# Kernel tuning notes

Measured on AMD Instinct MI355X. Metric: run time of the kernel, lower is better.

Reference implementation:

```python
import jax, jax.numpy as jnp
import numpy as np
import math

IMG = 640.0
SIZES = [32.0, 64.0, 128.0, 256.0]
STRIDES = [4, 8, 16, 32]
ARS = [0.5, 1.0, 2.0]
PRE_TOPK = 1000      # RPN_PRE_NMS_TOPK_TEST
POST_TOPK = 150      # RPN_POST_NMS_TOPK_TEST
NMS_THR = 0.7        # RPN_NMS_THRESHOLD
MIN_SIZE = 4.0       # MIN_BOX_SIZE
BBOX_CLAMP = math.log(1000.0 / 16.0)
ROI_OUT = 7          # ROI_OUTPUT_SIZE


def conv(x, w, b, pad):
    y = jax.lax.conv_general_dilated(x, w, (1, 1), [(pad, pad), (pad, pad)],
                                     dimension_numbers=('NCHW', 'OIHW', 'NCHW'))
    return y + b[None, :, None, None]


def level_anchors(H, W, stride, size):
    sx = (jnp.arange(W, dtype=jnp.float32) + 0.5) * stride
    sy = (jnp.arange(H, dtype=jnp.float32) + 0.5) * stride
    SY, SX = jnp.meshgrid(sy, sx, indexing='ij')
    shifts = jnp.stack([SX, SY, SX, SY], axis=-1).reshape(-1, 4)  # [H*W,4]
    base = []
    area = size * size
    for ar in ARS:
        w = math.sqrt(area / ar)
        h = ar * w
        base.append([-w / 2.0, -h / 2.0, w / 2.0, h / 2.0])
    base = jnp.asarray(base, jnp.float32)  # [3,4]
    return (shifts[:, None, :] + base[None, :, :]).reshape(-1, 4)  # [H*W*3,4]


def decode(deltas, boxes):
    w = jnp.maximum(boxes[:, 2] - boxes[:, 0], 1e-6)
    h = jnp.maximum(boxes[:, 3] - boxes[:, 1], 1e-6)
    cx = boxes[:, 0] + 0.5 * w
    cy = boxes[:, 1] + 0.5 * h
    dx, dy = deltas[:, 0], deltas[:, 1]
    dw = jnp.minimum(deltas[:, 2], BBOX_CLAMP)
    dh = jnp.minimum(deltas[:, 3], BBOX_CLAMP)
    pcx = cx + dx * w
    pcy = cy + dy * h
    pw = w * jnp.exp(dw)
    ph = h * jnp.exp(dh)
    return jnp.stack([pcx - 0.5 * pw, pcy - 0.5 * ph, pcx + 0.5 * pw, pcy + 0.5 * ph], axis=1)


def pairwise_iou(b):
    area = jnp.maximum(b[:, 2] - b[:, 0], 0) * jnp.maximum(b[:, 3] - b[:, 1], 0)
    lt = jnp.maximum(b[:, None, :2], b[None, :, :2])
    rb = jnp.minimum(b[:, None, 2:], b[None, :, 2:])
    wh = jnp.maximum(rb - lt, 0.0)
    inter = wh[..., 0] * wh[..., 1]
    return inter / jnp.maximum(area[:, None] + area[None, :] - inter, 1e-6)


def roi_align(feat, boxes, scale):
    # feat [C,H,W]; boxes [R,4] in image coords; one bilinear sample per bin center
    C, H, W = feat.shape
    b = boxes * scale
    x1, y1, x2, y2 = b[:, 0], b[:, 1], b[:, 2], b[:, 3]
    bw = jnp.maximum(x2 - x1, 1.0)
    bh = jnp.maximum(y2 - y1, 1.0)
    g = (jnp.arange(ROI_OUT, dtype=jnp.float32) + 0.5) / ROI_OUT
    px = x1[:, None] + g[None, :] * bw[:, None]   # [R,7]
    py = y1[:, None] + g[None, :] * bh[:, None]
    Y = jnp.broadcast_to(py[:, :, None], (py.shape[0], ROI_OUT, ROI_OUT))
    X = jnp.broadcast_to(px[:, None, :], (px.shape[0], ROI_OUT, ROI_OUT))
    y0f = jnp.floor(Y)
    x0f = jnp.floor(X)
    ly = Y - y0f
    lx = X - x0f
    y0 = jnp.clip(y0f, 0, H - 1).astype(jnp.int32)
    y1i = jnp.clip(y0f + 1, 0, H - 1).astype(jnp.int32)
    x0 = jnp.clip(x0f, 0, W - 1).astype(jnp.int32)
    x1i = jnp.clip(x0f + 1, 0, W - 1).astype(jnp.int32)
    f = lambda yi, xi: feat[:, yi, xi]  # [C,R,7,7]
    val = (f(y0, x0) * (1 - ly) * (1 - lx) + f(y0, x1i) * (1 - ly) * lx
           + f(y1i, x0) * ly * (1 - lx) + f(y1i, x1i) * ly * lx)
    return val.transpose(1, 0, 2, 3)  # [R,C,7,7]


def _forward(p2, p3, p4, p5, rpn_conv_w, rpn_conv_b, obj_w, obj_b, delta_w, delta_b,
             fc1_w, fc1_b, fc2_w, fc2_b, cls_w, cls_b, bbox_w, bbox_b):
    feats = [p2, p3, p4, p5]
    all_boxes, all_scores, all_lvl = [], [], []
    for lvl, (feat, stride, size) in enumerate(zip(feats, STRIDES, SIZES)):
        hid = jax.nn.relu(conv(feat, rpn_conv_w, rpn_conv_b, 1))
        obj = conv(hid, obj_w, obj_b, 0)      # [1,3,H,W]
        dlt = conv(hid, delta_w, delta_b, 0)  # [1,12,H,W]
        _, A, H, W = obj.shape
        scores = obj.transpose(0, 2, 3, 1).reshape(-1)  # [H*W*3]
        deltas = dlt.reshape(1, A, 4, H, W).transpose(0, 3, 4, 1, 2).reshape(-1, 4)
        anchors = level_anchors(H, W, stride, size)
        top_s, idx = jax.lax.top_k(scores, PRE_TOPK)
        boxes = jnp.clip(decode(deltas[idx], anchors[idx]), 0.0, IMG - 1.0)
        ww = boxes[:, 2] - boxes[:, 0]
        hh = boxes[:, 3] - boxes[:, 1]
        valid = (ww >= MIN_SIZE) & (hh >= MIN_SIZE)
        all_boxes.append(boxes)
        all_scores.append(jnp.where(valid, top_s, -1e30))
        all_lvl.append(jnp.full((PRE_TOPK,), float(lvl), jnp.float32))
    boxes = jnp.concatenate(all_boxes)   # [4000,4]
    scores = jnp.concatenate(all_scores)
    lvls = jnp.concatenate(all_lvl)
    N = boxes.shape[0]
    order = jnp.argsort(-scores)
    boxes_s = boxes[order]
    scores_s = scores[order]
    lvl_s = lvls[order]
    # batched NMS: offset per level so different levels never suppress each other
    off_boxes = boxes_s + (lvl_s * (IMG + 1.0) * 2.0)[:, None]
    iou = pairwise_iou(off_boxes)
    idx_r = jnp.arange(N)

    def body(i, keep):
        sup = (iou[i] > NMS_THR) & (idx_r > i) & keep[i]
        return keep & (~sup)

    keep = jax.lax.fori_loop(0, N, body, jnp.ones((N,), bool))
    kept_scores = jnp.where(keep, scores_s, -1e30)
    _, top_idx = jax.lax.top_k(kept_scores, POST_TOPK)
    props = boxes_s[top_idx]  # [150,4]
    # FPN level assignment (canonical formula) for ROI pooling
    pw = jnp.maximum(props[:, 2] - props[:, 0], 0.0)
    ph = jnp.maximum(props[:, 3] - props[:, 1], 0.0)
    k = jnp.clip(jnp.floor(4.0 + jnp.log2(jnp.sqrt(pw * ph) / 224.0 + 1e-6)), 2, 5)
    pooled = jnp.zeros((POST_TOPK, p2.shape[1], ROI_OUT, ROI_OUT), props.dtype)
    for lvl, (feat, stride) in enumerate(zip(feats, STRIDES)):
        pl = roi_align(feat[0], props, 1.0 / stride)
        pooled = pooled + jnp.where((k == (lvl + 2))[:, None, None, None], pl, 0.0)
    x = pooled.reshape(POST_TOPK, -1)            # [150, 12544]
    x = jax.nn.relu(x @ fc1_w.T + fc1_b)
    x = jax.nn.relu(x @ fc2_w.T + fc2_b)
    cls = x @ cls_w.T + cls_b                    # [150, 21]
    bbx = x @ bbox_w.T + bbox_b                  # [150, 84]
    return jnp.concatenate([cls, bbx], axis=-1)  # [150, 105]


def setup_inputs() -> dict:
    key = jax.random.key(0)
    ks = jax.random.split(key, 14)
    C = 256
    rn = lambda k, shape, s: jax.random.normal(k, shape, jnp.float32) * s
    return {
        'p2': rn(ks[0], (1, C, 160, 160), 0.5),
        'p3': rn(ks[1], (1, C, 80, 80), 0.5),
        'p4': rn(ks[2], (1, C, 40, 40), 0.5),
        'p5': rn(ks[3], (1, C, 20, 20), 0.5),
        'rpn_conv_w': rn(ks[4], (C, C, 3, 3), 0.01),
        'rpn_conv_b': jnp.zeros((C,), jnp.float32),
        'obj_w': rn(ks[5], (3, C, 1, 1), 0.01),
        'obj_b': jnp.zeros((3,), jnp.float32),
        'delta_w': rn(ks[6], (12, C, 1, 1), 0.01),
        'delta_b': jnp.zeros((12,), jnp.float32),
        'fc1_w': rn(ks[7], (1024, C * ROI_OUT * ROI_OUT), 0.01),
        'fc1_b': jnp.zeros((1024,), jnp.float32),
        'fc2_w': rn(ks[8], (1024, 1024), 0.01),
        'fc2_b': jnp.zeros((1024,), jnp.float32),
        'cls_w': rn(ks[9], (21, 1024), 0.01),
        'cls_b': jnp.zeros((21,), jnp.float32),
        'bbox_w': rn(ks[10], (84, 1024), 0.001),
        'bbox_b': jnp.zeros((84,), jnp.float32),
    }


def reference(p2, p3, p4, p5, rpn_conv_w, rpn_conv_b, obj_w, obj_b, delta_w, delta_b,
              fc1_w, fc1_b, fc2_w, fc2_b, cls_w, cls_b, bbox_w, bbox_b):
    return _forward(p2, p3, p4, p5, rpn_conv_w, rpn_conv_b, obj_w, obj_b, delta_w, delta_b,
                    fc1_w, fc1_b, fc2_w, fc2_b, cls_w, cls_b, bbox_w, bbox_b)
```

## Files before the change

kernel.cpp:

```cpp
#include <hip/hip_runtime.h>
#include <cstdint>

typedef unsigned long long u64;
typedef unsigned int u32;

__device__ inline u32 fmono(float f){ u32 u = __float_as_uint(f); u32 m = (u & 0x80000000u) ? 0xFFFFFFFFu : 0x80000000u; return u ^ m; }

__device__ const int    g_H[4]       = {160, 80, 40, 20};
__device__ const int    g_strideI[4] = {4, 8, 16, 32};
__device__ const float  g_size[4]    = {32.f, 64.f, 128.f, 256.f};
__device__ const int    g_cofs[4]    = {0, 76800, 96000, 100800};
__device__ const int    g_cnt[4]     = {76800, 19200, 4800, 1200};
__device__ const int    c_blkBase[5] = {0, 1600, 2000, 2288, 2416};
__device__ const int    c_S[4]       = {4, 4, 8, 8};
__device__ const int    c_pofs[4]    = {0, 25600, 32000, 33600};
__device__ const size_t c_partofs[4] = {0, 26214400, 32768000, 36044800};

__global__ __launch_bounds__(256) void wtr_k(const float* __restrict__ w, float* __restrict__ wT){
  __shared__ float tile[32][33];
  int tx = threadIdx.x & 31, ty = threadIdx.x >> 5;
  int row0 = blockIdx.x*32, co0 = blockIdx.y*32;
  #pragma unroll
  for (int r=0;r<4;r++){
    int co = co0 + ty + r*8;
    tile[ty+r*8][tx] = w[(size_t)co*2304 + row0 + tx];
  }
  __syncthreads();
  #pragma unroll
  for (int r=0;r<4;r++){
    int row = row0 + ty + r*8;
    wT[(size_t)row*256 + co0 + tx] = tile[tx][ty+r*8];
  }
}

__global__ void wcat_k(const float* __restrict__ cls_w, const float* __restrict__ cls_b,
                       const float* __restrict__ bbox_w, const float* __restrict__ bbox_b,
                       float* __restrict__ wcat, float* __restrict__ bcat){
  int t = blockIdx.x*256 + threadIdx.x;
  if (t < 105*1024){ int o = t >> 10, k = t & 1023; wcat[t] = (o < 21) ? cls_w[o*1024+k] : bbox_w[(o-21)*1024+k]; }
  if (t < 105) bcat[t] = (t < 21) ? cls_b[t] : bbox_b[t-21];
}

#define KC 4
__global__ __launch_bounds__(256) void rpn_conv_all_k(
    const float* __restrict__ p0, const float* __restrict__ p1,
    const float* __restrict__ p2f, const float* __restrict__ p3f,
    const float* __restrict__ wT, float* __restrict__ convp, int bidBase)
{
  int bid = blockIdx.x + bidBase;
  int lvl = (bid >= c_blkBase[1]) + (bid >= c_blkBase[2]) + (bid >= c_blkBase[3]);
  int local = bid - c_blkBase[lvl];
  int nz  = c_S[lvl];
  int H = g_H[lvl], W = H;
  const float* in = (lvl==0)?p0:((lvl==1)?p1:((lvl==2)?p2f:p3f));
  float* part = convp + c_partofs[lvl];
  int zb   = local % nz;
  int cb   = (local / nz) & 3;
  int tile = local / (nz*4);

  int tilesX = (W + 15) >> 4;
  int tr0 = (tile / tilesX) * 16;
  int tc0 = (tile % tilesX) * 16;
  int ciPer = 256 / nz;
  int ciBeg = zb * ciPer;
  int t   = threadIdx.x;
  int tco = t & 15, tp = t >> 4;
  int pr = (tp >> 2) * 4, pc = (tp & 3) * 4;
  int HW = H*W;

  __shared__ float sIn[KC][18][20];
  __shared__ float sW[KC*9][64];

  float* sInF = &sIn[0][0][0];
  float* sWF  = &sW[0][0];

  int   iOff[6]; int iLds[6]; bool iOk[6];
  #pragma unroll
  for (int s=0;s<6;s++){
    int e = t + s*256;
    bool a = (s<5) || (t < (KC*324 - 5*256));
    int ee = a ? e : 0;
    int c = ee/324, r2 = ee%324, row = r2/18, col = r2%18;
    int gy = tr0+row-1, gx = tc0+col-1;
    bool ok = a && ((unsigned)gy < (unsigned)H) && ((unsigned)gx < (unsigned)W);
    iOff[s] = c*HW + gy*W + gx;
    iLds[s] = c*360 + row*20 + col;
    iOk[s]  = ok;
  }
  bool iAct5 = (t < (KC*324 - 5*256));
  int wOff[3]; int wLds[3];
  #pragma unroll
  for (int s=0;s<3;s++){
    int e4 = t + s*256;
    bool a = (s<2) || (t < (KC*9*16 - 2*256));
    int ee = a ? e4 : 0;
    int row = ee>>4, c4 = (ee&15)<<2;
    wOff[s] = row*256 + cb*64 + c4;
    wLds[s] = row*64 + c4;
  }
  bool wAct2 = (t < (KC*9*16 - 2*256));

  float acc[4][16];
  #pragma unroll
  for (int o=0;o<4;o++)
    #pragma unroll
    for (int p=0;p<16;p++) acc[o][p]=0.f;

  float  ri0,ri1,ri2,ri3,ri4,ri5;
  float4 rw0,rw1,rw2;

  {
    const float* inb = in + (size_t)ciBeg*HW;
    const float* wb  = wT + (size_t)ciBeg*2304;
    ri0 = iOk[0] ? inb[iOff[0]] : 0.f;
    ri1 = iOk[1] ? inb[iOff[1]] : 0.f;
    ri2 = iOk[2] ? inb[iOff[2]] : 0.f;
    ri3 = iOk[3] ? inb[iOff[3]] : 0.f;
    ri4 = iOk[4] ? inb[iOff[4]] : 0.f;
    ri5 = iOk[5] ? inb[iOff[5]] : 0.f;
    rw0 = *(const float4*)&wb[wOff[0]];
    rw1 = *(const float4*)&wb[wOff[1]];
    if (wAct2) rw2 = *(const float4*)&wb[wOff[2]];
  }

  int ciEnd = ciBeg + ciPer;
  for (int ci0=ciBeg; ci0<ciEnd; ci0+=KC){
    sInF[iLds[0]] = ri0; sInF[iLds[1]] = ri1; sInF[iLds[2]] = ri2;
    sInF[iLds[3]] = ri3; sInF[iLds[4]] = ri4;
    if (iAct5) sInF[iLds[5]] = ri5;
    *(float4*)&sWF[wLds[0]] = rw0;
    *(float4*)&sWF[wLds[1]] = rw1;
    if (wAct2) *(float4*)&sWF[wLds[2]] = rw2;
    __syncthreads();

    if (ci0 + KC < ciEnd){
      const float* inb = in + (size_t)(ci0+KC)*HW;
      const float* wb  = wT + (size_t)(ci0+KC)*2304;
      ri0 = iOk[0] ? inb[iOff[0]] : 0.f;
      ri1 = iOk[1] ? inb[iOff[1]] : 0.f;
      ri2 = iOk[2] ? inb[iOff[2]] : 0.f;
      ri3 = iOk[3] ? inb[iOff[3]] : 0.f;
      ri4 = iOk[4] ? inb[iOff[4]] : 0.f;
      ri5 = iOk[5] ? inb[iOff[5]] : 0.f;
      rw0 = *(const float4*)&wb[wOff[0]];
      rw1 = *(const float4*)&wb[wOff[1]];
      if (wAct2) rw2 = *(const float4*)&wb[wOff[2]];
    }

    #pragma unroll
    for (int c=0;c<KC;c++){
      float rin[6][6];
      #pragma unroll
      for (int rr=0;rr<6;rr++){
        float4 a = *(const float4*)&sIn[c][pr+rr][pc];
        float2 b = *(const float2*)&sIn[c][pr+rr][pc+4];
        rin[rr][0]=a.x; rin[rr][1]=a.y; rin[rr][2]=a.z; rin[rr][3]=a.w;
        rin[rr][4]=b.x; rin[rr][5]=b.y;
      }
      #pragma unroll
      for (int k=0;k<9;k++){
        int ky=k/3, kx=k%3;
        float4 w0 = *(const float4*)&sW[c*9+k][tco*4];
        float wv[4] = {w0.x,w0.y,w0.z,w0.w};
        #pragma unroll
        for (int dr=0;dr<4;dr++)
          #pragma unroll
          for (int dc=0;dc<4;dc++){
            float iv = rin[dr+ky][dc+kx];
            int p = dr*4+dc;
            #pragma unroll
            for (int o=0;o<4;o++) acc[o][p] = fmaf(wv[o], iv, acc[o][p]);
          }
      }
    }
    __syncthreads();
  }

  int coBase = cb*64 + tco*4;
  float* pb = part + (size_t)zb*HW*256;
  #pragma unroll
  for (int dr=0;dr<4;dr++){
    int gy = tr0+pr+dr; if (gy>=H) continue;
    #pragma unroll
    for (int dc=0;dc<4;dc++){
      int gx = tc0+pc+dc; if (gx>=W) continue;
      int p = dr*4+dc;
      *(float4*)&pb[(size_t)(gy*W+gx)*256 + coBase] = make_float4(acc[0][p],acc[1][p],acc[2][p],acc[3][p]);
    }
  }
}

__global__ __launch_bounds__(256) void rpn_heads_k(
  const float* __restrict__ convp, const float* __restrict__ cbias,
  const float* __restrict__ ow, const float* __restrict__ ob,
  const float* __restrict__ dw, const float* __restrict__ db,
  float* __restrict__ scores, float* __restrict__ deltas)
{
  __shared__ float sw[15][256];
  int t = threadIdx.x;
  for (int e=t; e<15*256; e+=256){ int o=e>>8, k=e&255; sw[o][k] = (o<3)? ow[o*256+k] : dw[(o-3)*256+k]; }
  __syncthreads();
  int wv = t>>6, lane = t&63;
  float4 bv = *(const float4*)&cbias[lane*4];
  #pragma unroll
  for (int i=0;i<16;i++){
    int gpx = blockIdx.x*64 + wv*16 + i;
    if (gpx >= 34000) return;
    int lvl = (gpx >= 25600) + (gpx >= 32000) + (gpx >= 33600);
    int S = c_S[lvl];
    size_t stride = (size_t)g_H[lvl]*g_H[lvl]*256;
    const float* pb = convp + c_partofs[lvl] + (size_t)(gpx - c_pofs[lvl])*256 + lane*4;
    float vx=0.f, vy=0.f, vz=0.f, vw=0.f;
    for (int s=0;s<S;s++){
      float4 q = *(const float4*)(pb + (size_t)s*stride);
      vx += q.x; vy += q.y; vz += q.z; vw += q.w;
    }
    vx += bv.x; vy += bv.y; vz += bv.z; vw += bv.w;
    vx = vx>0.f?vx:0.f; vy = vy>0.f?vy:0.f; vz = vz>0.f?vz:0.f; vw = vw>0.f?vw:0.f;
    float a[15];
    #pragma unroll
    for (int o=0;o<15;o++){
      const float* w = &sw[o][lane*4];
      a[o] = w[0]*vx + w[1]*vy + w[2]*vz + w[3]*vw;
    }
    #pragma unroll
    for (int off=32; off; off>>=1)
      #pragma unroll
      for (int o=0;o<15;o++) a[o] += __shfl_xor(a[o], off, 64);
    if (lane==0){
      for (int q=0;q<3;q++) scores[gpx*3+q] = a[q] + ob[q];
      for (int q=0;q<3;q++)
        for (int j=0;j<4;j++)
          deltas[(size_t)(gpx*3+q)*4 + j] = a[3+q*4+j] + db[q*4+j];
    }
  }
}

__global__ __launch_bounds__(1024) void topk_k(
  const float* __restrict__ scores, float* __restrict__ top_s, u32* __restrict__ top_idx)
{
  int lvl = blockIdx.x;
  int base = g_cofs[lvl], N = g_cnt[lvl];
  const int K = 1000;
  __shared__ u32 hist[4096];
  __shared__ u64 sbuf[4096];
  __shared__ u32 shThr; __shared__ int scnt;
  int t = threadIdx.x;
  for (int e=t; e<4096; e+=1024) hist[e]=0;
  __syncthreads();
  for (int e=t; e<N; e+=1024){
    u32 m = fmono(scores[base+e]);
    atomicAdd(&hist[m>>20], 1u);
  }
  __syncthreads();
  if (t==0){
    int accu=0;
    for (int d=4095; d>=0; --d){
      int c = (int)hist[d];
      if (accu + c >= K){ shThr = (u32)d; break; }
      accu += c;
    }
    scnt = 0;
  }
  __syncthreads();
  u32 thr = shThr;
  for (int e=t; e<4096; e+=1024) sbuf[e]=0ull;
  __syncthreads();
  for (int e=t; e<N; e+=1024){
    u32 m = fmono(scores[base+e]);
    if ((m>>20) >= thr){
      int p = atomicAdd(&scnt, 1);
      if (p < 4096) sbuf[p] = ((u64)m << 32) | (u32)(~(u32)e);
    }
  }
  __syncthreads();
  for (int k=2;k<=4096;k<<=1)
    for (int j=k>>1;j>0;j>>=1){
      for (int i=t;i<4096;i+=1024){
        int ixj = i^j;
        if (ixj > i){
          u64 x = sbuf[i], y = sbuf[ixj];
          bool up = ((i & k) == 0);
          bool swp = up ? (x<y) : (x>y);
          if (swp){ sbuf[i]=y; sbuf[ixj]=x; }
        }
      }
      __syncthreads();
    }
  if (t<K){
    u64 key = sbuf[t];
    u32 idx = ~((u32)key);
    top_idx[lvl*1000+t] = idx;
    top_s[lvl*1000+t]   = scores[base + (int)idx];
  }
}

__global__ __launch_bounds__(1024) void sort_k(const u32* __restrict__ top_idx, const float* __restrict__ top_s,
  const float* __restrict__ deltas,
  float* __restrict__ cat_sc, float4* __restrict__ cat_bx,
  float* __restrict__ scores_s, float4* __restrict__ boxes_s, float4* __restrict__ obox)
{
  int t = threadIdx.x;
  for (int e=t; e<4000; e+=1024){
    int lvl = e/1000;
    u32 idx = top_idx[e];
    float score = top_s[e];
    int W = g_H[lvl];
    int strd = g_strideI[lvl];
    float size = g_size[lvl];
    int a = (int)(idx % 3u); int pix = (int)(idx / 3u);
    int px = pix % W, py = pix / W;
    double area = (double)size*(double)size;
    double ar = (a==0)?0.5:((a==1)?1.0:2.0);
    double wd = sqrt(area/ar);
    double hd = ar*wd;
    float bx1 = (float)(-wd*0.5), by1 = (float)(-hd*0.5), bx2=(float)(wd*0.5), by2=(float)(hd*0.5);
    float sx = ((float)px + 0.5f)*(float)strd;
    float sy = ((float)py + 0.5f)*(float)strd;
    float ax1 = sx+bx1, ay1=sy+by1, ax2=sx+bx2, ay2=sy+by2;
    float w = fmaxf(ax2-ax1, 1e-6f), h = fmaxf(ay2-ay1, 1e-6f);
    float cx = ax1 + 0.5f*w, cy = ay1 + 0.5f*h;
    const float* d = &deltas[(size_t)(g_cofs[lvl] + (int)idx)*4];
    float dx = d[0], dy = d[1];
    float dwv = fminf(d[2], 4.135166556742356f);
    float dhv = fminf(d[3], 4.135166556742356f);
    float pcx = cx + dx*w, pcy = cy + dy*h;
    float pw = w*expf(dwv), ph = h*expf(dhv);
    float x1 = pcx - 0.5f*pw, y1 = pcy - 0.5f*ph, x2 = pcx + 0.5f*pw, y2 = pcy + 0.5f*ph;
    x1 = fminf(fmaxf(x1,0.f),639.f); y1 = fminf(fmaxf(y1,0.f),639.f);
    x2 = fminf(fmaxf(x2,0.f),639.f); y2 = fminf(fmaxf(y2,0.f),639.f);
    bool valid = ((x2-x1) >= 4.f) && ((y2-y1) >= 4.f);
    cat_bx[e] = make_float4(x1,y1,x2,y2);
    cat_sc[e] = valid ? score : -1e30f;
  }
  __syncthreads();
  __shared__ u64 s[4096];
  for (int i=t;i<4096;i+=1024){
    u64 key = 0;
    if (i<4000) key = ((u64)fmono(cat_sc[i])<<32) | (u32)(~(u32)i);
    s[i]=key;
  }
  __syncthreads();
  for (int k=2;k<=4096;k<<=1)
    for (int j=k>>1;j>0;j>>=1){
      for (int i=t;i<4096;i+=1024){
        int ixj=i^j;
        if (ixj>i){
          u64 x=s[i], y=s[ixj];
          bool up = ((i&k)==0);
          bool swp = up ? (x<y):(x>y);
          if (swp){ s[i]=y; s[ixj]=x; }
        }
      }
      __syncthreads();
    }
  for (int r=t;r<4000;r+=1024){
    u32 o = ~((u32)s[r]);
    float4 b = cat_bx[o];
    scores_s[r] = cat_sc[o];
    boxes_s[r] = b;
    float off = (float)(o/1000u) * 1282.0f;
    obox[r] = make_float4(b.x+off, b.y+off, b.z+off, b.w+off);
  }
}

__global__ __launch_bounds__(256) void iou_k(const float4* __restrict__ obox, u64* __restrict__ mask)
{
  int w = threadIdx.x;
  int i = blockIdx.x*4 + threadIdx.y;
  if (i >= 4000 || w >= 63) return;
  float4 bi = obox[i];
  float ai = fmaxf(bi.z-bi.x,0.f)*fmaxf(bi.w-bi.y,0.f);
  u64 bits=0;
  int c0=w*64;
  for (int l=0;l<64;l++){
    int c=c0+l;
    if (c>=4000) break;
    if (c<=i) continue;
    float4 bc = obox[c];
    float ac = fmaxf(bc.z-bc.x,0.f)*fmaxf(bc.w-bc.y,0.f);
    float ltx = fmaxf(bi.x, bc.x), lty = fmaxf(bi.y, bc.y);
    float rbx = fminf(bi.z, bc.z), rby = fminf(bi.w, bc.w);
    float wx = fmaxf(rbx-ltx,0.f), wy = fmaxf(rby-lty,0.f);
    float inter = wx*wy;
    float uni = fmaxf(ai+ac-inter, 1e-6f);
    if (inter/uni > 0.7f) bits |= (1ull<<l);
  }
  mask[(size_t)i*63 + w] = bits;
}

#define PF 32
__global__ __launch_bounds__(64) void nms_scan_k(const u64* __restrict__ mask,
   const float* __restrict__ scores_s, const float4* __restrict__ boxes_s, float4* __restrict__ props)
{
  int lane = threadIdx.x;
  bool act = lane < 63;
  const u64* mrow = mask + lane;
  u64 removed = 0;

  u64 bufA[PF], bufB[PF];
  #pragma unroll
  for (int j=0;j<PF;j++) bufA[j] = act ? mrow[(size_t)j*63] : 0ull;

  const int NG = 4000/PF;
  for (int g=0; g<NG; g+=2){
    if (g+1 < NG){
      #pragma unroll
      for (int j=0;j<PF;j++) bufB[j] = act ? mrow[(size_t)((g+1)*PF+j)*63] : 0ull;
    }
    #pragma unroll
    for (int j=0;j<PF;j++){
      int i = g*PF + j;
      u64 rm = __shfl(removed, i>>6, 64);
      bool keep = ((rm >> (i&63)) & 1ull) == 0ull;
      if (keep) removed |= bufA[j];
    }
    if (g+2 < NG){
      #pragma unroll
      for (int j=0;j<PF;j++) bufA[j] = act ? mrow[(size_t)((g+2)*PF+j)*63] : 0ull;
    }
    if (g+1 < NG){
      #pragma unroll
      for (int j=0;j<PF;j++){
        int i = (g+1)*PF + j;
        u64 rm = __shfl(removed, i>>6, 64);
        bool keep = ((rm >> (i&63)) & 1ull) == 0ull;
        if (keep) removed |= bufB[j];
      }
    }
  }

  u64 keepbits = ~removed;
  u64 selbits = 0;
  if (act){
    #pragma unroll
    for (int j=0;j<64;j++){
      int i = lane*64 + j;
      if (i < 4000 && ((keepbits>>j)&1ull) && scores_s[i] > -1e29f) selbits |= (1ull<<j);
    }
  }
  u64 validbits = 0;
  if (act){
    int nvalid = 4000 - lane*64;
    if (nvalid >= 64) validbits = ~0ull;
    else if (nvalid > 0) validbits = (1ull<<nvalid) - 1ull;
  }
  u64 nonbits = (~selbits) & validbits;

  int cntSel = __popcll(selbits);
  int incS = cntSel;
  #pragma unroll
  for (int off2=1; off2<64; off2<<=1){ int v = __shfl_up(incS, off2, 64); if (lane>=off2) incS += v; }
  int exSel = incS - cntSel;
  int totalSel = __shfl(incS, 63, 64);
  int cnt = totalSel < 150 ? totalSel : 150;

  int cntNon = __popcll(nonbits);
  int incN = cntNon;
  #pragma unroll
  for (int off2=1; off2<64; off2<<=1){ int v = __shfl_up(incN, off2, 64); if (lane>=off2) incN += v; }
  int exNon = incN - cntNon;

  if (act){
    int r = exSel;
    #pragma unroll
    for (int j=0;j<64;j++){
      if ((selbits>>j)&1ull){
        if (r < 150) props[r] = boxes_s[lane*64 + j];
        r++;
      }
    }
    int r2 = cnt + exNon;
    #pragma unroll
    for (int j=0;j<64;j++){
      if ((nonbits>>j)&1ull){
        if (r2 < 150) props[r2] = boxes_s[lane*64 + j];
        r2++;
      }
    }
  }
}

__global__ __launch_bounds__(256) void roi_k(const float* __restrict__ p2, const float* __restrict__ p3,
  const float* __restrict__ p4, const float* __restrict__ p5, const float4* __restrict__ props, float* __restrict__ x0)
{
  int roi = blockIdx.y, p = blockIdx.x, c = threadIdx.x;
  float4 b = props[roi];
  float pw = fmaxf(b.z-b.x, 0.f), ph = fmaxf(b.w-b.y, 0.f);
  float kf = floorf(4.f + log2f(sqrtf(pw*ph)/224.f + 1e-6f));
  kf = fminf(fmaxf(kf, 2.f), 5.f);
  int lvl = (int)kf - 2;
  const float* f = (lvl==0)?p2:((lvl==1)?p3:((lvl==2)?p4:p5));
  int H = g_H[lvl]; int HW = H*H;
  float scale = 1.f/(float)g_strideI[lvl];
  float x1 = b.x*scale, y1 = b.y*scale, x2 = b.z*scale, y2 = b.w*scale;
  float bw = fmaxf(x2-x1, 1.f), bh = fmaxf(y2-y1, 1.f);
  int py = p/7, px = p%7;
  float gx = ((float)px + 0.5f)/7.f;
  float gy = ((float)py + 0.5f)/7.f;
  float X = x1 + gx*bw;
  float Y = y1 + gy*bh;
  float x0f = floorf(X), y0f = floorf(Y);
  float lx = X - x0f, ly = Y - y0f;
  int xi0 = (int)fminf(fmaxf(x0f,0.f),(float)(H-1));
  int xi1 = (int)fminf(fmaxf(x0f+1.f,0.f),(float)(H-1));
  int yi0 = (int)fminf(fmaxf(y0f,0.f),(float)(H-1));
  int yi1 = (int)fminf(fmaxf(y0f+1.f,0.f),(float)(H-1));
  float v00 = f[(size_t)c*HW + yi0*H + xi0];
  float v01 = f[(size_t)c*HW + yi0*H + xi1];
  float v10 = f[(size_t)c*HW + yi1*H + xi0];
  float v11 = f[(size_t)c*HW + yi1*H + xi1];
  float val = v00*(1.f-ly)*(1.f-lx) + v01*(1.f-ly)*lx + v10*ly*(1.f-lx) + v11*ly*lx;
  x0[(size_t)roi*12544 + c*49 + p] = val;
}

__global__ __launch_bounds__(256) void fc_split_k(const float* __restrict__ X, const float* __restrict__ Wt,
  float* __restrict__ partial, int M, int N, int K, int KS)
{
  __shared__ float sx[32][33];
  __shared__ float sw[32][64];
  int t = threadIdx.x;
  int tn = t & 15, tm = t >> 4;
  int nb = blockIdx.x, mb = blockIdx.y, zb = blockIdx.z;
  int row0 = mb*32 + tm*2, col0 = nb*64 + tn*4;
  int kbeg = zb*KS, kend = kbeg + KS;
  float acc[2][4] = {{0,0,0,0},{0,0,0,0}};
  int wn = t & 63, kg = t >> 6;
  for (int k0=kbeg;k0<kend;k0+=32){
    for (int e=t;e<1024;e+=256){
      int m=e>>5, kk=e&31;
      int row=mb*32+m;
      sx[m][kk] = (row<M)? X[(size_t)row*K + k0+kk] : 0.f;
    }
    int co = nb*64+wn;
    if (co<N){
      const float* wp = &Wt[(size_t)co*K + k0 + kg*8];
      float4 va = *(const float4*)wp;
      float4 vb = *(const float4*)(wp+4);
      sw[kg*8+0][wn]=va.x; sw[kg*8+1][wn]=va.y; sw[kg*8+2][wn]=va.z; sw[kg*8+3][wn]=va.w;
      sw[kg*8+4][wn]=vb.x; sw[kg*8+5][wn]=vb.y; sw[kg*8+6][wn]=vb.z; sw[kg*8+7][wn]=vb.w;
    } else {
      #pragma unroll
      for (int j=0;j<8;j++) sw[kg*8+j][wn]=0.f;
    }
    __syncthreads();
    #pragma unroll 8
    for (int kk=0;kk<32;kk++){
      float xa = sx[tm*2+0][kk], xb = sx[tm*2+1][kk];
      float4 wv = *(const float4*)&sw[kk][tn*4];
      acc[0][0]=fmaf(xa,wv.x,acc[0][0]); acc[0][1]=fmaf(xa,wv.y,acc[0][1]);
      acc[0][2]=fmaf(xa,wv.z,acc[0][2]); acc[0][3]=fmaf(xa,wv.w,acc[0][3]);
      acc[1][0]=fmaf(xb,wv.x,acc[1][0]); acc[1][1]=fmaf(xb,wv.y,acc[1][1]);
      acc[1][2]=fmaf(xb,wv.z,acc[1][2]); acc[1][3]=fmaf(xb,wv.w,acc[1][3]);
    }
    __syncthreads();
  }
  for (int dm=0;dm<2;dm++){
    int row=row0+dm; if (row>=M) continue;
    for (int dn=0;dn<4;dn++){
      int col=col0+dn; if (col>=N) continue;
      partial[((size_t)zb*M + row)*N + col] = acc[dm][dn];
    }
  }
}

__global__ __launch_bounds__(256) void fc_reduce_k(const float* __restrict__ partial, const float* __restrict__ bias,
  float* __restrict__ Y, int M, int N, int S, int dorelu)
{
  int idx = blockIdx.x*256 + threadIdx.x;
  if (idx >= M*N) return;
  int col = idx % N;
  float v = bias[col];
  size_t stride = (size_t)M*N;
  for (int s=0;s<S;s++) v += partial[s*stride + idx];
  if (dorelu) v = fmaxf(v, 0.f);
  Y[idx] = v;
}

extern "C" void kernel_launch(void* const* d_in, const int* in_sizes, int n_in,
                              void* d_out, int out_size, void* d_ws, size_t ws_size,
                              hipStream_t stream)
{
  (void)in_sizes; (void)n_in; (void)out_size; (void)ws_size;
  const float* p[4] = {(const float*)d_in[0], (const float*)d_in[1], (const float*)d_in[2], (const float*)d_in[3]};
  const float* rpn_w = (const float*)d_in[4];
  const float* rpn_b = (const float*)d_in[5];
  const float* obj_w = (const float*)d_in[6];
  const float* obj_b = (const float*)d_in[7];
  const float* del_w = (const float*)d_in[8];
  const float* del_b = (const float*)d_in[9];
  const float* fc1_w = (const float*)d_in[10];
  const float* fc1_b = (const float*)d_in[11];
  const float* fc2_w = (const float*)d_in[12];
  const float* fc2_b = (const float*)d_in[13];
  const float* cls_w = (const float*)d_in[14];
  const float* cls_b = (const float*)d_in[15];
  const float* bbox_w= (const float*)d_in[16];
  const float* bbox_b= (const float*)d_in[17];

  char* ws = (char*)d_ws;
  size_t off = 0;
  auto alloc = [&](size_t bytes){ size_t o = off; off += (bytes + 255) & ~(size_t)255; return o; };
  float*  wT1      = (float*)(ws + alloc(589824ull*4));
  float*  hid      = (float*)(ws + alloc(34000ull*256*4));
  float*  scores   = (float*)(ws + alloc(102000ull*4));
  float*  deltas   = (float*)(ws + alloc(102000ull*16));
  float*  top_s    = (float*)(ws + alloc(4000ull*4));
  u32*    top_idx  = (u32*)  (ws + alloc(4000ull*4));
  float*  cat_sc   = (float*)(ws + alloc(4000ull*4));
  float4* cat_bx   = (float4*)(ws + alloc(4000ull*16));
  float*  scores_s = (float*)(ws + alloc(4000ull*4));
  float4* boxes_s  = (float4*)(ws + alloc(4000ull*16));
  float4* obox     = (float4*)(ws + alloc(4000ull*16));
  u64*    mask     = (u64*)  (ws + alloc(4000ull*63*8));
  float4* props    = (float4*)(ws + alloc(150ull*16));
  float*  x0       = (float*)(ws + alloc(150ull*12544*4));
  float*  x1       = (float*)(ws + alloc(150ull*1024*4));
  float*  x2       = (float*)(ws + alloc(150ull*1024*4));
  float*  wcat     = (float*)(ws + alloc(105ull*1024*4));
  float*  bcat     = (float*)(ws + alloc(105ull*4));
  float*  convp    = (float*)(ws + alloc(36864000ull*4));
  float*  partial  = hid;

  hipLaunchKernelGGL(wtr_k, dim3(72,8), dim3(256), 0, stream, rpn_w, wT1);
  hipLaunchKernelGGL(wcat_k, dim3((105*1024+255)/256), dim3(256), 0, stream, cls_w, cls_b, bbox_w, bbox_b, wcat, bcat);

  hipLaunchKernelGGL(rpn_conv_all_k, dim3(1208), dim3(256), 0, stream,
                     p[0], p[1], p[2], p[3], wT1, convp, 0);
  hipLaunchKernelGGL(rpn_conv_all_k, dim3(1208), dim3(256), 0, stream,
                     p[0], p[1], p[2], p[3], wT1, convp, 1208);

  hipLaunchKernelGGL(rpn_heads_k, dim3((34000+63)/64), dim3(256), 0, stream,
                     convp, rpn_b, obj_w, obj_b, del_w, del_b, scores, deltas);
  hipLaunchKernelGGL(topk_k, dim3(4), dim3(1024), 0, stream, scores, top_s, top_idx);
  hipLaunchKernelGGL(sort_k, dim3(1), dim3(1024), 0, stream, top_idx, top_s, deltas,
                     cat_sc, cat_bx, scores_s, boxes_s, obox);
  hipLaunchKernelGGL(iou_k, dim3(1000), dim3(64,4), 0, stream, obox, mask);
  hipLaunchKernelGGL(nms_scan_k, dim3(1), dim3(64), 0, stream, mask, scores_s, boxes_s, props);
  hipLaunchKernelGGL(roi_k, dim3(49,150), dim3(256), 0, stream, p[0],p[1],p[2],p[3], props, x0);

  hipLaunchKernelGGL(fc_split_k, dim3(16,5,28), dim3(256), 0, stream, x0, fc1_w, partial, 150, 1024, 12544, 448);
  hipLaunchKernelGGL(fc_reduce_k, dim3((150*1024+255)/256), dim3(256), 0, stream, partial, fc1_b, x1, 150, 1024, 28, 1);
  hipLaunchKernelGGL(fc_split_k, dim3(16,5,8), dim3(256), 0, stream, x1, fc2_w, partial, 150, 1024, 1024, 128);
  hipLaunchKernelGGL(fc_reduce_k, dim3((150*1024+255)/256), dim3(256), 0, stream, partial, fc2_b, x2, 150, 1024, 8, 1);
  hipLaunchKernelGGL(fc_split_k, dim3(2,5,8), dim3(256), 0, stream, x2, wcat, partial, 150, 105, 1024, 128);
  hipLaunchKernelGGL(fc_reduce_k, dim3((150*105+255)/256), dim3(256), 0, stream, partial, bcat, (float*)d_out, 150, 105, 8, 0);
}
```

Measured before the change: 1.380 ms.

## Resolve NMS keep bits per 64-row block with one shuffle instead of per-row shuffles

The serial NMS scan now handles the suppression mask in 64-row blocks aligned to word boundaries. Every lane resolves that block's keep decisions locally from its own removed word, and the result from the lane owning the block is broadcast with a single shuffle. Each lane then ORs in the mask rows that were kept. This replaces one cross-lane shuffle per candidate row with one per block. The cost is roughly twice the ALU work and 128 u64 prefetch registers per lane, which may raise register pressure or cause spills.

```diff
diff --git a/kernel.cpp b/kernel.cpp
--- a/kernel.cpp
+++ b/kernel.cpp
@@ -389,7 +389,6 @@
   mask[(size_t)i*63 + w] = bits;
 }
 
-#define PF 32
 __global__ __launch_bounds__(64) void nms_scan_k(const u64* __restrict__ mask,
    const float* __restrict__ scores_s, const float4* __restrict__ boxes_s, float4* __restrict__ props)
 {
@@ -398,34 +397,55 @@
   const u64* mrow = mask + lane;
   u64 removed = 0;
 
-  u64 bufA[PF], bufB[PF];
-  #pragma unroll
-  for (int j=0;j<PF;j++) bufA[j] = act ? mrow[(size_t)j*63] : 0ull;
-
-  const int NG = 4000/PF;
+  const int NG = 63;
+  u64 bufA[64], bufB[64];
+  #pragma unroll
+  for (int j=0;j<64;j++){
+    int i = j;
+    bufA[j] = (act && i < 4000) ? mrow[(size_t)i*63] : 0ull;
+  }
+
   for (int g=0; g<NG; g+=2){
     if (g+1 < NG){
       #pragma unroll
-      for (int j=0;j<PF;j++) bufB[j] = act ? mrow[(size_t)((g+1)*PF+j)*63] : 0ull;
-    }
-    #pragma unroll
-    for (int j=0;j<PF;j++){
-      int i = g*PF + j;
-      u64 rm = __shfl(removed, i>>6, 64);
-      bool keep = ((rm >> (i&63)) & 1ull) == 0ull;
-      if (keep) removed |= bufA[j];
+      for (int j=0;j<64;j++){
+        int i = (g+1)*64 + j;
+        bufB[j] = (act && i < 4000) ? mrow[(size_t)i*63] : 0ull;
+      }
+    }
+    {
+      u64 rm = removed, kb = 0;
+      #pragma unroll
+      for (int j=0;j<64;j++){
+        u64 bit = 1ull<<j;
+        bool keep = ((rm & bit) == 0ull);
+        if (keep){ kb |= bit; rm |= bufA[j]; }
+      }
+      kb = __shfl(kb, g, 64);
+      #pragma unroll
+      for (int j=0;j<64;j++){
+        if ((kb >> j) & 1ull) removed |= bufA[j];
+      }
     }
     if (g+2 < NG){
       #pragma unroll
-      for (int j=0;j<PF;j++) bufA[j] = act ? mrow[(size_t)((g+2)*PF+j)*63] : 0ull;
+      for (int j=0;j<64;j++){
+        int i = (g+2)*64 + j;
+        bufA[j] = (act && i < 4000) ? mrow[(size_t)i*63] : 0ull;
+      }
     }
     if (g+1 < NG){
-      #pragma unroll
-      for (int j=0;j<PF;j++){
-        int i = (g+1)*PF + j;
-        u64 rm = __shfl(removed, i>>6, 64);
-        bool keep = ((rm >> (i&63)) & 1ull) == 0ull;
-        if (keep) removed |= bufB[j];
+      u64 rm = removed, kb = 0;
+      #pragma unroll
+      for (int j=0;j<64;j++){
+        u64 bit = 1ull<<j;
+        bool keep = ((rm & bit) == 0ull);
+        if (keep){ kb |= bit; rm |= bufB[j]; }
+      }
+      kb = __shfl(kb, g+1, 64);
+      #pragma unroll
+      for (int j=0;j<64;j++){
+        if ((kb >> j) & 1ull) removed |= bufB[j];
       }
     }
   }
```

Result: faster. 1.347 ms (-2.4%).
